# Performance work log

Measured on AMD Instinct MI355X. Metric: run time of the kernel, lower is better.

Reference implementation:

```python
import jax, jax.numpy as jnp
import numpy as np

B, S, D, H = 8, 1024, 256, 16
HD = D // H  # head_dim = 16
THETA = 10000.0


def rope(x):
    # Faithful to RotaryEmbeddings: integer-division exponent, 1-indexed
    # positions, rotor = sin + i*cos (real part is sin).
    b, s, d = x.shape
    i = jnp.arange(0, d, 2)
    expo = (2 * i) // d  # integer division: 0 for first half, 1 for second
    thetas = 1.0 / (THETA ** expo.astype(jnp.float32))  # [d/2]
    pos = jnp.arange(s, dtype=jnp.float32) + 1.0  # 1-indexed positions
    ang = pos[:, None] * thetas[None, :]  # [s, d/2]
    sin, cos = jnp.sin(ang), jnp.cos(ang)
    xp = x.reshape(b, s, d // 2, 2)
    xe, xo = xp[..., 0], xp[..., 1]  # consecutive pairs (view_as_complex)
    # (xe + i*xo) * (sin + i*cos)
    real = xe * sin - xo * cos
    imag = xe * cos + xo * sin
    return jnp.stack((real, imag), axis=-1).reshape(b, s, d)


def setup_inputs() -> dict:
    key = jax.random.key(0)
    ks = jax.random.split(key, 9)
    sc = 1.0 / np.sqrt(D)
    return {
        "x": jax.random.normal(ks[0], (B, S, D), dtype=jnp.float32),
        "wq_w": jax.random.normal(ks[1], (D, D), dtype=jnp.float32) * sc,
        "wq_b": jax.random.normal(ks[2], (D,), dtype=jnp.float32) * 0.01,
        "wk_w": jax.random.normal(ks[3], (D, D), dtype=jnp.float32) * sc,
        "wk_b": jax.random.normal(ks[4], (D,), dtype=jnp.float32) * 0.01,
        "wv_w": jax.random.normal(ks[5], (D, D), dtype=jnp.float32) * sc,
        "wv_b": jax.random.normal(ks[6], (D,), dtype=jnp.float32) * 0.01,
        "wo_w": jax.random.normal(ks[7], (D, D), dtype=jnp.float32) * sc,
        "wo_b": jax.random.normal(ks[8], (D,), dtype=jnp.float32) * 0.01,
    }


def reference(x, wq_w, wq_b, wk_w, wk_b, wv_w, wv_b, wo_w, wo_b):
    b, s, d = x.shape
    q = x @ wq_w.T + wq_b
    k = x @ wk_w.T + wk_b  # computed in original but dead in no-cache path
    v = x @ wv_w.T + wv_b
    del k
    xq = rope(q).reshape(b, s, H, HD).transpose(0, 2, 1, 3)  # [b,h,s,hd]
    xv = rope(v).reshape(b, s, H, HD).transpose(0, 2, 1, 3)  # [b,h,s,hd]
    # no-cache path: keys = xq (rotated queries), values = rotated v; NO softmax
    scores = jnp.einsum('bhqd,bhkd->bhqk', xq, xq) / jnp.sqrt(jnp.float32(HD))
    att = jnp.einsum('bhqk,bhkd->bhqd', scores, xv)  # [b,h,s,hd]
    att = att.transpose(0, 2, 1, 3).reshape(b, s, d)
    return att @ wo_w.T + wo_b
```

## Files before the change

kernel.cpp:

```cpp
#include <hip/hip_runtime.h>
#include <math.h>

#define Gz 8192
#define Dz 256
#define Sz 1024

typedef _Float16 half8 __attribute__((ext_vector_type(8)));
typedef float    floatx4 __attribute__((ext_vector_type(4)));

__global__ __launch_bounds__(256) void qv_gemm_rope(
    const float* __restrict__ x,
    const float* __restrict__ Wq, const float* __restrict__ bq,
    const float* __restrict__ Wv, const float* __restrict__ bv,
    _Float16* __restrict__ xq, _Float16* __restrict__ xv)
{
    __shared__ __align__(16) _Float16 As[64][40];
    __shared__ __align__(16) _Float16 Bs[64][40];
    const int t    = threadIdx.x;
    const int lane = t & 63;
    const int w    = t >> 6;
    const int g0   = blockIdx.x * 64;
    const int n0   = blockIdx.y * 64;
    const float* W    = blockIdx.z ? Wv : Wq;
    const float* bias = blockIdx.z ? bv : bq;
    _Float16*    outp = blockIdx.z ? xv : xq;

    const int srow = t >> 2;
    const int skg  = t & 3;

    floatx4 acc[4] = {};

    const int fr = lane & 15;
    const int kq = lane >> 4;

    for (int k0 = 0; k0 < Dz; k0 += 32) {
        const float* xg = &x[(size_t)(g0 + srow) * Dz + k0 + skg * 8];
        const float* wg = &W[(size_t)(n0 + srow) * Dz + k0 + skg * 8];
        float4 xa = ((const float4*)xg)[0], xb = ((const float4*)xg)[1];
        float4 wa = ((const float4*)wg)[0], wb = ((const float4*)wg)[1];
        half8 ha, hb;
        ha[0]=(_Float16)xa.x; ha[1]=(_Float16)xa.y; ha[2]=(_Float16)xa.z; ha[3]=(_Float16)xa.w;
        ha[4]=(_Float16)xb.x; ha[5]=(_Float16)xb.y; ha[6]=(_Float16)xb.z; ha[7]=(_Float16)xb.w;
        hb[0]=(_Float16)wa.x; hb[1]=(_Float16)wa.y; hb[2]=(_Float16)wa.z; hb[3]=(_Float16)wa.w;
        hb[4]=(_Float16)wb.x; hb[5]=(_Float16)wb.y; hb[6]=(_Float16)wb.z; hb[7]=(_Float16)wb.w;
        __syncthreads();
        *(half8*)&As[srow][skg * 8] = ha;
        *(half8*)&Bs[srow][skg * 8] = hb;
        __syncthreads();
        half8 afrag = *(const half8*)&As[w * 16 + fr][kq * 8];
        #pragma unroll
        for (int j = 0; j < 4; ++j) {
            half8 bfrag = *(const half8*)&Bs[j * 16 + fr][kq * 8];
            acc[j] = __builtin_amdgcn_mfma_f32_16x16x32_f16(afrag, bfrag, acc[j], 0, 0, 0);
        }
    }

    #pragma unroll
    for (int j = 0; j < 4; ++j) {
        const int c = n0 + j * 16 + fr;
        const float bcol  = bias[c];
        const float theta = ((c >> 1) < 64) ? 1.0f : 1e-4f;
        const float sign  = (c & 1) ? 1.0f : -1.0f;
        #pragma unroll
        for (int i = 0; i < 4; ++i) {
            const int g = g0 + w * 16 + kq * 4 + i;
            float v = acc[j][i] + bcol;
            float other = __shfl_xor(v, 1, 64);
            float ang = (float)((g & (Sz - 1)) + 1) * theta;
            float sn, cs;
            sincosf(ang, &sn, &cs);
            outp[(size_t)g * Dz + c] = (_Float16)(v * sn + sign * other * cs);
        }
    }
}

__global__ __launch_bounds__(256) void head_outer(
    const _Float16* __restrict__ xq, const _Float16* __restrict__ xv,
    float* __restrict__ M)
{
    __shared__ __align__(16) _Float16 qsT[16][136];
    __shared__ __align__(16) _Float16 vsT[16][136];
    const int t  = threadIdx.x;
    const int bh = blockIdx.x;
    const int b  = bh >> 4, h = bh & 15;
    const size_t base = (size_t)b * Sz * Dz + (size_t)blockIdx.y * 128 * Dz + h * 16;

    {
        const int s = t >> 1, eg = t & 1;
        half8 q8 = *(const half8*)&xq[base + (size_t)s * Dz + eg * 8];
        half8 v8 = *(const half8*)&xv[base + (size_t)s * Dz + eg * 8];
        #pragma unroll
        for (int i = 0; i < 8; ++i) {
            qsT[eg * 8 + i][s] = q8[i];
            vsT[eg * 8 + i][s] = v8[i];
        }
    }
    __syncthreads();

    const int e = t >> 4, f = t & 15;
    float acc = 0.f;
    #pragma unroll
    for (int s0 = 0; s0 < 128; s0 += 8) {
        half8 q8 = *(const half8*)&qsT[e][s0];
        half8 v8 = *(const half8*)&vsT[f][s0];
        #pragma unroll
        for (int i = 0; i < 8; ++i) acc += (float)q8[i] * (float)v8[i];
    }
    atomicAdd(&M[(size_t)bh * 256 + t], acc * 0.25f);
}

__global__ __launch_bounds__(256) void make_p(
    const float* __restrict__ M, const float* __restrict__ Wo,
    _Float16* __restrict__ Pt)
{
    __shared__ float Ms[256];
    const int t  = threadIdx.x;
    const int bh = blockIdx.x;
    const int b  = bh >> 4, h = bh & 15;
    Ms[t] = M[(size_t)bh * 256 + t];
    __syncthreads();

    const int c = t;
    float wo[16];
    const float4* wop = (const float4*)&Wo[(size_t)c * Dz + h * 16];
    #pragma unroll
    for (int q = 0; q < 4; ++q) {
        float4 v = wop[q];
        wo[4*q+0] = v.x; wo[4*q+1] = v.y; wo[4*q+2] = v.z; wo[4*q+3] = v.w;
    }
    half8 lo, hi;
    #pragma unroll
    for (int e = 0; e < 16; ++e) {
        float a = 0.f;
        #pragma unroll
        for (int f = 0; f < 16; ++f) a = fmaf(Ms[e * 16 + f], wo[f], a);
        if (e < 8) lo[e] = (_Float16)a; else hi[e - 8] = (_Float16)a;
    }
    _Float16* dst = &Pt[((size_t)(b * 256 + c)) * Dz + h * 16];
    *(half8*)dst       = lo;
    *(half8*)(dst + 8) = hi;
}

__global__ __launch_bounds__(256) void out_gemm(
    const _Float16* __restrict__ xq, const _Float16* __restrict__ Pt,
    const float* __restrict__ bo, float* __restrict__ out)
{
    __shared__ __align__(16) _Float16 As[64][40];
    __shared__ __align__(16) _Float16 Bs[64][40];
    const int t    = threadIdx.x;
    const int lane = t & 63;
    const int w    = t >> 6;
    const int g0   = blockIdx.x * 64;
    const int n0   = blockIdx.y * 64;
    const int b    = g0 >> 10;

    const int srow = t >> 2;
    const int skg  = t & 3;
    const int fr   = lane & 15;
    const int kq   = lane >> 4;

    floatx4 acc[4] = {};

    for (int k0 = 0; k0 < Dz; k0 += 32) {
        half8 ha = *(const half8*)&xq[(size_t)(g0 + srow) * Dz + k0 + skg * 8];
        half8 hb = *(const half8*)&Pt[((size_t)(b * 256 + n0 + srow)) * Dz + k0 + skg * 8];
        __syncthreads();
        *(half8*)&As[srow][skg * 8] = ha;
        *(half8*)&Bs[srow][skg * 8] = hb;
        __syncthreads();
        half8 afrag = *(const half8*)&As[w * 16 + fr][kq * 8];
        #pragma unroll
        for (int j = 0; j < 4; ++j) {
            half8 bfrag = *(const half8*)&Bs[j * 16 + fr][kq * 8];
            acc[j] = __builtin_amdgcn_mfma_f32_16x16x32_f16(afrag, bfrag, acc[j], 0, 0, 0);
        }
    }

    #pragma unroll
    for (int j = 0; j < 4; ++j) {
        const int c = n0 + j * 16 + fr;
        const float bcol = bo[c];
        #pragma unroll
        for (int i = 0; i < 4; ++i) {
            const int g = g0 + w * 16 + kq * 4 + i;
            out[(size_t)g * Dz + c] = acc[j][i] + bcol;
        }
    }
}

extern "C" void kernel_launch(void* const* d_in, const int* in_sizes, int n_in,
                              void* d_out, int out_size, void* d_ws, size_t ws_size,
                              hipStream_t stream)
{
    const float* x    = (const float*)d_in[0];
    const float* wq_w = (const float*)d_in[1];
    const float* wq_b = (const float*)d_in[2];
    const float* wv_w = (const float*)d_in[5];
    const float* wv_b = (const float*)d_in[6];
    const float* wo_w = (const float*)d_in[7];
    const float* wo_b = (const float*)d_in[8];

    _Float16* xq16 = (_Float16*)d_ws;
    _Float16* xv16 = xq16 + (size_t)Gz * Dz;
    _Float16* Pt   = xv16 + (size_t)Gz * Dz;
    float*    M    = (float*)(Pt + (size_t)8 * 256 * 256);
    float*    out  = (float*)d_out;

    hipMemsetAsync(M, 0, 128 * 256 * sizeof(float), stream);
    qv_gemm_rope<<<dim3(Gz / 64, Dz / 64, 2), 256, 0, stream>>>(
        x, wq_w, wq_b, wv_w, wv_b, xq16, xv16);
    head_outer<<<dim3(128, 8), 256, 0, stream>>>(xq16, xv16, M);
    make_p<<<dim3(128), 256, 0, stream>>>(M, wo_w, Pt);
    out_gemm<<<dim3(Gz / 64, Dz / 64), 256, 0, stream>>>(xq16, Pt, wo_b, out);
}
```

Before: 103.5 us.

## Pre-convert inputs to fp16, enlarge GEMM tiles with direct global-to-LDS loads

Adds a separate conversion kernel that casts x and the Wq/Wv weights to fp16 once. The QV GEMM then uses 128x128 tiles with 64-wide k steps, loads tiles straight into LDS through global_load_lds, and computes fast sincos once per row. The output GEMM is retiled to 64x128 with the same load path. The atomic reduction and memset are replaced by per-chunk partial buffers that make_p sums. This trades an extra launch and an extra round trip of the fp16 copy through memory for better data reuse per block. The unpadded LDS layout may cause bank conflicts, and the approximate sincos may lose accuracy.

Result: no change. 102.7 us, median of 2 (-0.8%).

```diff
diff --git a/kernel.cpp b/kernel.cpp
--- a/kernel.cpp
+++ b/kernel.cpp
@@ -1,5 +1,4 @@
 #include <hip/hip_runtime.h>
-#include <math.h>
 
 #define Gz 8192
 #define Dz 256
@@ -8,81 +7,121 @@
 typedef _Float16 half8 __attribute__((ext_vector_type(8)));
 typedef float    floatx4 __attribute__((ext_vector_type(4)));
 
+#define GLOAD_LDS(gptr, lptr)                                                      \
+    __builtin_amdgcn_global_load_lds(                                              \
+        (const __attribute__((address_space(1))) void*)(gptr),                     \
+        (__attribute__((address_space(3))) void*)(lptr), 16, 0, 0)
+
+__device__ inline half8 cvt8(const float* __restrict__ p) {
+    float4 a = ((const float4*)p)[0];
+    float4 b = ((const float4*)p)[1];
+    half8 h;
+    h[0]=(_Float16)a.x; h[1]=(_Float16)a.y; h[2]=(_Float16)a.z; h[3]=(_Float16)a.w;
+    h[4]=(_Float16)b.x; h[5]=(_Float16)b.y; h[6]=(_Float16)b.z; h[7]=(_Float16)b.w;
+    return h;
+}
+
+__global__ __launch_bounds__(256) void convert_kernel(
+    const float* __restrict__ x, const float* __restrict__ wq,
+    const float* __restrict__ wv,
+    _Float16* __restrict__ x16, _Float16* __restrict__ w16)
+{
+    size_t e = ((size_t)blockIdx.x * 256 + threadIdx.x) * 8;
+    const float* src;
+    _Float16* dst;
+    if (e < (size_t)Gz * Dz) { src = x + e; dst = x16 + e; }
+    else {
+        size_t e2 = e - (size_t)Gz * Dz;
+        dst = w16 + e2;
+        src = (e2 < 65536) ? (wq + e2) : (wv + (e2 - 65536));
+    }
+    *(half8*)dst = cvt8(src);
+}
+
 __global__ __launch_bounds__(256) void qv_gemm_rope(
-    const float* __restrict__ x,
-    const float* __restrict__ Wq, const float* __restrict__ bq,
-    const float* __restrict__ Wv, const float* __restrict__ bv,
+    const _Float16* __restrict__ x16, const _Float16* __restrict__ w16,
+    const float* __restrict__ bq, const float* __restrict__ bv,
     _Float16* __restrict__ xq, _Float16* __restrict__ xv)
 {
-    __shared__ __align__(16) _Float16 As[64][40];
-    __shared__ __align__(16) _Float16 Bs[64][40];
-    const int t    = threadIdx.x;
-    const int lane = t & 63;
-    const int w    = t >> 6;
-    const int g0   = blockIdx.x * 64;
-    const int n0   = blockIdx.y * 64;
-    const float* W    = blockIdx.z ? Wv : Wq;
-    const float* bias = blockIdx.z ? bv : bq;
-    _Float16*    outp = blockIdx.z ? xv : xq;
-
-    const int srow = t >> 2;
-    const int skg  = t & 3;
-
-    floatx4 acc[4] = {};
-
-    const int fr = lane & 15;
-    const int kq = lane >> 4;
-
-    for (int k0 = 0; k0 < Dz; k0 += 32) {
-        const float* xg = &x[(size_t)(g0 + srow) * Dz + k0 + skg * 8];
-        const float* wg = &W[(size_t)(n0 + srow) * Dz + k0 + skg * 8];
-        float4 xa = ((const float4*)xg)[0], xb = ((const float4*)xg)[1];
-        float4 wa = ((const float4*)wg)[0], wb = ((const float4*)wg)[1];
-        half8 ha, hb;
-        ha[0]=(_Float16)xa.x; ha[1]=(_Float16)xa.y; ha[2]=(_Float16)xa.z; ha[3]=(_Float16)xa.w;
-        ha[4]=(_Float16)xb.x; ha[5]=(_Float16)xb.y; ha[6]=(_Float16)xb.z; ha[7]=(_Float16)xb.w;
-        hb[0]=(_Float16)wa.x; hb[1]=(_Float16)wa.y; hb[2]=(_Float16)wa.z; hb[3]=(_Float16)wa.w;
-        hb[4]=(_Float16)wb.x; hb[5]=(_Float16)wb.y; hb[6]=(_Float16)wb.z; hb[7]=(_Float16)wb.w;
-        __syncthreads();
-        *(half8*)&As[srow][skg * 8] = ha;
-        *(half8*)&Bs[srow][skg * 8] = hb;
-        __syncthreads();
-        half8 afrag = *(const half8*)&As[w * 16 + fr][kq * 8];
-        #pragma unroll
-        for (int j = 0; j < 4; ++j) {
-            half8 bfrag = *(const half8*)&Bs[j * 16 + fr][kq * 8];
-            acc[j] = __builtin_amdgcn_mfma_f32_16x16x32_f16(afrag, bfrag, acc[j], 0, 0, 0);
-        }
-    }
+    __shared__ _Float16 As[128 * 64];
+    __shared__ _Float16 Bs[128 * 64];
+    const int t = threadIdx.x, lane = t & 63, w = t >> 6;
+    const int g0 = blockIdx.x * 128;
+    const int by = blockIdx.y;
+    const int n0 = by * 128;
+    const int wm = (w >> 1) * 64, wn = (w & 1) * 64;
+    const int fr = lane & 15, kq = lane >> 4;
+
+    floatx4 acc[4][4] = {};
+
+    for (int k0 = 0; k0 < Dz; k0 += 64) {
+        __syncthreads();
+        #pragma unroll
+        for (int p = 0; p < 4; ++p) {
+            const int flat = (t + 256 * p) * 8;
+            const int row = flat >> 6, col = flat & 63;
+            GLOAD_LDS(x16 + (size_t)(g0 + row) * Dz + k0 + col, &As[flat]);
+            GLOAD_LDS(w16 + (size_t)(n0 + row) * Dz + k0 + col, &Bs[flat]);
+        }
+        __syncthreads();
+        #pragma unroll
+        for (int ks = 0; ks < 2; ++ks) {
+            const int kk = ks * 32 + kq * 8;
+            half8 a[4], b[4];
+            #pragma unroll
+            for (int i = 0; i < 4; ++i) a[i] = *(const half8*)&As[(wm + i * 16 + fr) * 64 + kk];
+            #pragma unroll
+            for (int j = 0; j < 4; ++j) b[j] = *(const half8*)&Bs[(wn + j * 16 + fr) * 64 + kk];
+            #pragma unroll
+            for (int i = 0; i < 4; ++i)
+                #pragma unroll
+                for (int j = 0; j < 4; ++j)
+                    acc[i][j] = __builtin_amdgcn_mfma_f32_16x16x32_f16(a[i], b[j], acc[i][j], 0, 0, 0);
+        }
+    }
+
+    const int qside = (by < 2);
+    const float* bias = qside ? bq : bv;
+    _Float16* outp = qside ? xq : xv;
+    const float theta = (by & 1) ? 1e-4f : 1.0f;
+    const float sign  = (fr & 1) ? 1.0f : -1.0f;
+
+    float sn[4][4], cs[4][4];
+    #pragma unroll
+    for (int i = 0; i < 4; ++i)
+        #pragma unroll
+        for (int r = 0; r < 4; ++r) {
+            const int g = g0 + wm + i * 16 + kq * 4 + r;
+            const float pos = (float)((g & (Sz - 1)) + 1);
+            __sincosf(pos * theta, &sn[i][r], &cs[i][r]);
+        }
 
     #pragma unroll
     for (int j = 0; j < 4; ++j) {
-        const int c = n0 + j * 16 + fr;
-        const float bcol  = bias[c];
-        const float theta = ((c >> 1) < 64) ? 1.0f : 1e-4f;
-        const float sign  = (c & 1) ? 1.0f : -1.0f;
-        #pragma unroll
-        for (int i = 0; i < 4; ++i) {
-            const int g = g0 + w * 16 + kq * 4 + i;
-            float v = acc[j][i] + bcol;
-            float other = __shfl_xor(v, 1, 64);
-            float ang = (float)((g & (Sz - 1)) + 1) * theta;
-            float sn, cs;
-            sincosf(ang, &sn, &cs);
-            outp[(size_t)g * Dz + c] = (_Float16)(v * sn + sign * other * cs);
-        }
+        const int ch = (by & 1) * 128 + wn + j * 16 + fr;
+        const float bcol = bias[ch];
+        #pragma unroll
+        for (int i = 0; i < 4; ++i)
+            #pragma unroll
+            for (int r = 0; r < 4; ++r) {
+                const int g = g0 + wm + i * 16 + kq * 4 + r;
+                float v = acc[i][j][r] + bcol;
+                float other = __shfl_xor(v, 1, 64);
+                outp[(size_t)g * Dz + ch] =
+                    (_Float16)(v * sn[i][r] + sign * other * cs[i][r]);
+            }
     }
 }
 
 __global__ __launch_bounds__(256) void head_outer(
     const _Float16* __restrict__ xq, const _Float16* __restrict__ xv,
-    float* __restrict__ M)
+    float* __restrict__ Mpart)
 {
     __shared__ __align__(16) _Float16 qsT[16][136];
     __shared__ __align__(16) _Float16 vsT[16][136];
-    const int t  = threadIdx.x;
+    const int t = threadIdx.x;
     const int bh = blockIdx.x;
-    const int b  = bh >> 4, h = bh & 15;
+    const int b = bh >> 4, h = bh & 15;
     const size_t base = (size_t)b * Sz * Dz + (size_t)blockIdx.y * 128 * Dz + h * 16;
 
     {
@@ -106,18 +145,21 @@
         #pragma unroll
         for (int i = 0; i < 8; ++i) acc += (float)q8[i] * (float)v8[i];
     }
-    atomicAdd(&M[(size_t)bh * 256 + t], acc * 0.25f);
+    Mpart[((size_t)blockIdx.y * 128 + bh) * 256 + t] = acc;
 }
 
 __global__ __launch_bounds__(256) void make_p(
-    const float* __restrict__ M, const float* __restrict__ Wo,
+    const float* __restrict__ Mpart, const float* __restrict__ Wo,
     _Float16* __restrict__ Pt)
 {
     __shared__ float Ms[256];
-    const int t  = threadIdx.x;
+    const int t = threadIdx.x;
     const int bh = blockIdx.x;
-    const int b  = bh >> 4, h = bh & 15;
-    Ms[t] = M[(size_t)bh * 256 + t];
+    const int b = bh >> 4, h = bh & 15;
+    float s = 0.f;
+    #pragma unroll
+    for (int c = 0; c < 8; ++c) s += Mpart[((size_t)c * 128 + bh) * 256 + t];
+    Ms[t] = s * 0.25f;
     __syncthreads();
 
     const int c = t;
@@ -145,46 +187,60 @@
     const _Float16* __restrict__ xq, const _Float16* __restrict__ Pt,
     const float* __restrict__ bo, float* __restrict__ out)
 {
-    __shared__ __align__(16) _Float16 As[64][40];
-    __shared__ __align__(16) _Float16 Bs[64][40];
-    const int t    = threadIdx.x;
-    const int lane = t & 63;
-    const int w    = t >> 6;
-    const int g0   = blockIdx.x * 64;
-    const int n0   = blockIdx.y * 64;
-    const int b    = g0 >> 10;
-
-    const int srow = t >> 2;
-    const int skg  = t & 3;
-    const int fr   = lane & 15;
-    const int kq   = lane >> 4;
-
-    floatx4 acc[4] = {};
-
-    for (int k0 = 0; k0 < Dz; k0 += 32) {
-        half8 ha = *(const half8*)&xq[(size_t)(g0 + srow) * Dz + k0 + skg * 8];
-        half8 hb = *(const half8*)&Pt[((size_t)(b * 256 + n0 + srow)) * Dz + k0 + skg * 8];
-        __syncthreads();
-        *(half8*)&As[srow][skg * 8] = ha;
-        *(half8*)&Bs[srow][skg * 8] = hb;
-        __syncthreads();
-        half8 afrag = *(const half8*)&As[w * 16 + fr][kq * 8];
-        #pragma unroll
-        for (int j = 0; j < 4; ++j) {
-            half8 bfrag = *(const half8*)&Bs[j * 16 + fr][kq * 8];
-            acc[j] = __builtin_amdgcn_mfma_f32_16x16x32_f16(afrag, bfrag, acc[j], 0, 0, 0);
+    __shared__ _Float16 As[64 * 64];
+    __shared__ _Float16 Bs[128 * 64];
+    const int t = threadIdx.x, lane = t & 63, w = t >> 6;
+    const int g0 = blockIdx.x * 64;
+    const int n0 = blockIdx.y * 128;
+    const int b  = g0 >> 10;
+    const int wm = (w >> 1) * 32, wn = (w & 1) * 64;
+    const int fr = lane & 15, kq = lane >> 4;
+    const _Float16* Pb = Pt + (size_t)b * 256 * Dz;
+
+    floatx4 acc[2][4] = {};
+
+    for (int k0 = 0; k0 < Dz; k0 += 64) {
+        __syncthreads();
+        #pragma unroll
+        for (int p = 0; p < 2; ++p) {
+            const int flat = (t + 256 * p) * 8;
+            const int row = flat >> 6, col = flat & 63;
+            GLOAD_LDS(xq + (size_t)(g0 + row) * Dz + k0 + col, &As[flat]);
+        }
+        #pragma unroll
+        for (int p = 0; p < 4; ++p) {
+            const int flat = (t + 256 * p) * 8;
+            const int row = flat >> 6, col = flat & 63;
+            GLOAD_LDS(Pb + (size_t)(n0 + row) * Dz + k0 + col, &Bs[flat]);
+        }
+        __syncthreads();
+        #pragma unroll
+        for (int ks = 0; ks < 2; ++ks) {
+            const int kk = ks * 32 + kq * 8;
+            half8 a[2], bf[4];
+            #pragma unroll
+            for (int i = 0; i < 2; ++i) a[i] = *(const half8*)&As[(wm + i * 16 + fr) * 64 + kk];
+            #pragma unroll
+            for (int j = 0; j < 4; ++j) bf[j] = *(const half8*)&Bs[(wn + j * 16 + fr) * 64 + kk];
+            #pragma unroll
+            for (int i = 0; i < 2; ++i)
+                #pragma unroll
+                for (int j = 0; j < 4; ++j)
+                    acc[i][j] = __builtin_amdgcn_mfma_f32_16x16x32_f16(a[i], bf[j], acc[i][j], 0, 0, 0);
         }
     }
 
     #pragma unroll
     for (int j = 0; j < 4; ++j) {
-        const int c = n0 + j * 16 + fr;
+        const int c = n0 + wn + j * 16 + fr;
         const float bcol = bo[c];
         #pragma unroll
-        for (int i = 0; i < 4; ++i) {
-            const int g = g0 + w * 16 + kq * 4 + i;
-            out[(size_t)g * Dz + c] = acc[j][i] + bcol;
-        }
+        for (int i = 0; i < 2; ++i)
+            #pragma unroll
+            for (int r = 0; r < 4; ++r) {
+                const int g = g0 + wm + i * 16 + kq * 4 + r;
+                out[(size_t)g * Dz + c] = acc[i][j][r] + bcol;
+            }
     }
 }
 
@@ -200,16 +256,19 @@
     const float* wo_w = (const float*)d_in[7];
     const float* wo_b = (const float*)d_in[8];
 
-    _Float16* xq16 = (_Float16*)d_ws;
+    _Float16* x16  = (_Float16*)d_ws;
+    _Float16* w16  = x16  + (size_t)Gz * Dz;
+    _Float16* xq16 = w16  + 131072;
     _Float16* xv16 = xq16 + (size_t)Gz * Dz;
     _Float16* Pt   = xv16 + (size_t)Gz * Dz;
-    float*    M    = (float*)(Pt + (size_t)8 * 256 * 256);
+    float*    Mpart = (float*)(Pt + 524288);
     float*    out  = (float*)d_out;
 
-    hipMemsetAsync(M, 0, 128 * 256 * sizeof(float), stream);
-    qv_gemm_rope<<<dim3(Gz / 64, Dz / 64, 2), 256, 0, stream>>>(
-        x, wq_w, wq_b, wv_w, wv_b, xq16, xv16);
-    head_outer<<<dim3(128, 8), 256, 0, stream>>>(xq16, xv16, M);
-    make_p<<<dim3(128), 256, 0, stream>>>(M, wo_w, Pt);
-    out_gemm<<<dim3(Gz / 64, Dz / 64), 256, 0, stream>>>(xq16, Pt, wo_b, out);
-}
+    convert_kernel<<<dim3((Gz * Dz + 131072) / 2048), 256, 0, stream>>>(
+        x, wq_w, wv_w, x16, w16);
+    qv_gemm_rope<<<dim3(Gz / 128, 4), 256, 0, stream>>>(
+        x16, w16, wq_b, wv_b, xq16, xv16);
+    head_outer<<<dim3(128, 8), 256, 0, stream>>>(xq16, xv16, Mpart);
+    make_p<<<dim3(128), 256, 0, stream>>>(Mpart, wo_w, Pt);
+    out_gemm<<<dim3(Gz / 64, 2), 256, 0, stream>>>(xq16, Pt, wo_b, out);
+}
```
